# Kernel tuning notes

Measured on AMD Instinct MI355X. Metric: run time of the kernel, lower is better.

## Reference

```python
import jax, jax.numpy as jnp
import numpy as np
from jax import lax

D, NH, T, DFF, SD = 8, 4, 60, 2048, 17
DH = D // NH
NEG = -1e9

def _ln(x, g, b, eps=1e-5):
    m = jnp.mean(x, -1, keepdims=True)
    v = jnp.mean((x - m) ** 2, -1, keepdims=True)
    return (x - m) / jnp.sqrt(v + eps) * g + b

def _mha(q_in, k_in, v_in, Wqkv, bqkv, Wo, bo, mask):
    Wq, Wk, Wv = jnp.split(Wqkv, 3, axis=0)
    bq, bk, bv = jnp.split(bqkv, 3)
    def proj(x, W, bb):
        B, S, _ = x.shape
        return (x @ W.T + bb).reshape(B, S, NH, DH).transpose(0, 2, 1, 3)
    q = proj(q_in, Wq, bq); k = proj(k_in, Wk, bk); v = proj(v_in, Wv, bv)
    s = jnp.einsum('bhqd,bhkd->bhqk', q, k) / np.float32(np.sqrt(DH))
    s = jnp.where(mask, NEG, s)
    o = jnp.einsum('bhqk,bhkd->bhqd', jax.nn.softmax(s, axis=-1), v)
    B, _, S, _ = o.shape
    return o.transpose(0, 2, 1, 3).reshape(B, S, D) @ Wo.T + bo

def _ffn(x, W1, b1, W2, b2):
    return jax.nn.relu(x @ W1.T + b1) @ W2.T + b2

def _forward(x, emb_W, emb_b, eqW, eqb, eoW, eob, ef1W, ef1b, ef2W, ef2b, el1g, el1b, el2g, el2b, eng, enb, dsqW, dsqb, dsoW, dsob, dcqW, dcqb, dcoW, dcob, df1W, df1b, df2W, df2b, dl1g, dl1b, dl2g, dl2b, dl3g, dl3b, dng, dnb, fc_W, fc_b):
    B = x.shape[0]
    idx = jnp.arange(T)
    causal = (idx[None, :] > idx[:, None])[None, None]  # [1,1,T,T], True = blocked

    @jax.checkpoint
    def step(buf, t):
        keymask = (idx > t)[None, None, None, :]  # positions beyond t are padding
        mem = buf
        for i in range(6):  # nn.Transformer default encoder layers
            mem = _ln(mem + _mha(mem, mem, mem, eqW[i], eqb[i], eoW[i], eob[i], keymask), el1g[i], el1b[i])
            mem = _ln(mem + _ffn(mem, ef1W[i], ef1b[i], ef2W[i], ef2b[i]), el2g[i], el2b[i])
        mem = _ln(mem, eng, enb)
        y = buf
        for i in range(2):  # decoder layers
            y = _ln(y + _mha(y, y, y, dsqW[i], dsqb[i], dsoW[i], dsob[i], causal), dl1g[i], dl1b[i])
            y = _ln(y + _mha(y, mem, mem, dcqW[i], dcqb[i], dcoW[i], dcob[i], keymask), dl2g[i], dl2b[i])
            y = _ln(y + _ffn(y, df1W[i], df1b[i], df2W[i], df2b[i]), dl3g[i], dl3b[i])
        y = _ln(y, dng, dnb)
        st = jnp.take(y, t, axis=1) @ fc_W.T + fc_b  # decoded state at last valid pos [B,17]
        buf = buf.at[:, t + 1].set(st @ emb_W.T + emb_b, mode='drop')
        return buf, st

    buf0 = jnp.zeros((B, T, D), x.dtype).at[:, 0].set(x)
    _, states = lax.scan(step, buf0, idx)
    return jnp.transpose(states, (1, 0, 2))  # [B, T, state_dim]

def setup_inputs() -> dict:
    B = 128
    keys = iter(jax.random.split(jax.random.key(0), 64))
    def W(shape):
        return jax.random.normal(next(keys), shape, jnp.float32) / np.float32(np.sqrt(shape[-1]))
    z = lambda *s: jnp.zeros(s, jnp.float32)
    o = lambda *s: jnp.ones(s, jnp.float32)
    return dict(
        quantized_eos_embedding=jax.random.normal(next(keys), (B, D), jnp.float32),
        emb_W=W((D, SD)), emb_b=z(D),
        eqW=W((6, 3 * D, D)), eqb=z(6, 3 * D), eoW=W((6, D, D)), eob=z(6, D),
        ef1W=W((6, DFF, D)), ef1b=z(6, DFF), ef2W=W((6, D, DFF)), ef2b=z(6, D),
        el1g=o(6, D), el1b=z(6, D), el2g=o(6, D), el2b=z(6, D), eng=o(D), enb=z(D),
        dsqW=W((2, 3 * D, D)), dsqb=z(2, 3 * D), dsoW=W((2, D, D)), dsob=z(2, D),
        dcqW=W((2, 3 * D, D)), dcqb=z(2, 3 * D), dcoW=W((2, D, D)), dcob=z(2, D),
        df1W=W((2, DFF, D)), df1b=z(2, DFF), df2W=W((2, D, DFF)), df2b=z(2, D),
        dl1g=o(2, D), dl1b=z(2, D), dl2g=o(2, D), dl2b=z(2, D), dl3g=o(2, D), dl3b=z(2, D),
        dng=o(D), dnb=z(D),
        fc_W=W((SD, D)), fc_b=z(SD),
    )

def reference(quantized_eos_embedding, emb_W, emb_b, eqW, eqb, eoW, eob, ef1W, ef1b, ef2W, ef2b, el1g, el1b, el2g, el2b, eng, enb, dsqW, dsqb, dsoW, dsob, dcqW, dcqb, dcoW, dcob, df1W, df1b, df2W, df2b, dl1g, dl1b, dl2g, dl2b, dl3g, dl3b, dng, dnb, fc_W, fc_b):
    return _forward(quantized_eos_embedding, emb_W, emb_b, eqW, eqb, eoW, eob, ef1W, ef1b, ef2W, ef2b, el1g, el1b, el2g, el2b, eng, enb, dsqW, dsqb, dsoW, dsob, dcqW, dcqb, dcoW, dcob, df1W, df1b, df2W, df2b, dl1g, dl1b, dl2g, dl2b, dl3g, dl3b, dng, dnb, fc_W, fc_b)
```

## Files before the change

### kernel.cpp

```cpp
#include <hip/hip_runtime.h>


typedef __attribute__((ext_vector_type(8))) short short8;
typedef __attribute__((ext_vector_type(4))) float floatx4;
typedef __attribute__((ext_vector_type(4))) unsigned uint4v;

#define DEV static __device__ __forceinline__

namespace {
constexpr int D   = 8;
constexpr int T   = 60;
constexpr int DFF = 2048;
constexpr int SD  = 17;
constexpr int NT  = 512;
constexpr int NW  = NT / 64;
constexpr int NBLK = DFF / 32;
constexpr int BPW  = NBLK / NW;
constexpr int LSTR = NBLK * 2048;
}

struct Params { const float* in[39]; float* out; };

DEV unsigned short f2bf(float f) {
  unsigned u = __builtin_bit_cast(unsigned, f);
  return (unsigned short)((u + 0x8000u) >> 16);
}
DEV float bf2f(unsigned short h) {
  unsigned u = ((unsigned)h) << 16;
  return __builtin_bit_cast(float, u);
}
DEV floatx4 mfma16(short8 a, short8 b, floatx4 c) {
  return __builtin_amdgcn_mfma_f32_16x16x32_bf16(a, b, c, 0, 0, 0);
}
DEV unsigned cvtpk(float lo, float hi) {
  unsigned r;
  asm("v_cvt_pk_bf16_f32 %0, %1, %2" : "=v"(r) : "v"(lo), "v"(hi));
  return r;
}
DEV float lo2f(unsigned u) { return __builtin_bit_cast(float, u << 16); }
DEV float hi2f(unsigned u) { return __builtin_bit_cast(float, u & 0xffff0000u); }
DEV short8 pack4(unsigned a, unsigned b, unsigned c, unsigned d) {
  uint4v u = {a, b, c, d};
  return __builtin_bit_cast(short8, u);
}

__global__ __launch_bounds__(64) void repack_kernel(Params P, short* ws) {
  const int wg = blockIdx.x;
  const int L = wg >> 6, blk = wg & 63;
  const int l = (int)threadIdx.x, gg = l >> 4, rr = l & 15;
  const float *W1p, *b1p, *W2p;
  if (L < 6) { W1p = P.in[7] + L * 16384;  b1p = P.in[8] + L * 2048;  W2p = P.in[9] + L * 16384; }
  else { int m = L - 6; W1p = P.in[25] + m * 16384; b1p = P.in[26] + m * 2048; W2p = P.in[27] + m * 16384; }
  short* out = ws + (L * 64 + blk) * 2048;
  const int j0 = blk * 32;
  short8 z = {0,0,0,0,0,0,0,0};
  for (int tt = 0; tt < 2; ++tt) {
    int j = j0 + tt * 16 + rr;
    short8 r = z;
    if (gg == 3) {
      unsigned short h = f2bf(b1p[j]);
      r[0] = (short)h; r[1] = (short)f2bf(b1p[j] - bf2f(h));
    } else {
      const float* p = W1p + j * 8;
#pragma unroll
      for (int i = 0; i < 8; ++i) {
        float v = p[i];
        unsigned short h = f2bf(v);
        r[i] = (short)((gg == 1) ? f2bf(v - bf2f(h)) : h);
      }
    }
    *(short8*)(out + tt * 512 + l * 8) = r;
  }
  short8 wh = z, wl = z;
  if (rr < 8) {
#pragma unroll
    for (int i = 0; i < 8; ++i) {
      int j = j0 + (i < 4 ? gg * 4 + i : 16 + gg * 4 + (i - 4));
      float v = W2p[rr * 2048 + j];
      unsigned short h = f2bf(v);
      wh[i] = (short)h;
      wl[i] = (short)f2bf(v - bf2f(h));
    }
  }
  *(short8*)(out + 1024 + l * 8) = wh;
  *(short8*)(out + 1536 + l * 8) = wl;
}

__global__ __launch_bounds__(NT, 2) void tdec_kernel(Params P, const short* ws) {
  const int b    = blockIdx.x;
  const int tid  = (int)threadIdx.x;
  const int lane = tid & 63;
  const int wave = tid >> 6;
  const int gg   = lane >> 4;
  const int rr   = lane & 15;

  __shared__ float buf[T][D];
  __shared__ __align__(16) float X[64][D];
  __shared__ float Mem[64][D];
  __shared__ float Qs[64][D];
  __shared__ float Ks[64][D];
  __shared__ float Vs[64][D];
  __shared__ float ATT[64][D];
  __shared__ __align__(16) float red[NW * 1024];
  __shared__ float wAll[10 * 288];
  __shared__ float lnp[40][D];
  __shared__ float b2all[8][D];
  __shared__ float fcw[SD][D];
  __shared__ float fcbv[SD];
  __shared__ float embw[D][SD];
  __shared__ float embbv[D];
  __shared__ float stv[SD];

  for (int o = tid; o < 2880; o += NT) {
    int a = o / 288, off = o - a * 288;
    const float *Wq, *Bq, *Wo, *Bo; int li;
    if (a < 6)              { li = a;            Wq=P.in[3];  Bq=P.in[4];  Wo=P.in[5];  Bo=P.in[6];  }
    else if (((a - 6) & 1) == 0) { li = (a-6)>>1; Wq=P.in[17]; Bq=P.in[18]; Wo=P.in[19]; Bo=P.in[20]; }
    else                    { li = (a-6)>>1;     Wq=P.in[21]; Bq=P.in[22]; Wo=P.in[23]; Bo=P.in[24]; }
    float v;
    if (off < 192)      v = Wq[li*192 + off];
    else if (off < 216) v = Bq[li*24  + off - 192];
    else if (off < 280) v = Wo[li*64  + off - 216];
    else                v = Bo[li*8   + off - 280];
    wAll[o] = v;
  }
  for (int o = tid; o < 320; o += NT) {
    int row = o >> 3, k = o & 7;
    const float* src;
    if (row < 24) { int li = row >> 2, w = row & 3;
      src = (w==0 ? P.in[11] : w==1 ? P.in[12] : w==2 ? P.in[13] : P.in[14]) + li*8;
    } else if (row < 26) src = (row == 24 ? P.in[15] : P.in[16]);
    else if (row < 38) { int q = row - 26, li = q / 6, w = q - li*6;
      src = (w==0?P.in[29]:w==1?P.in[30]:w==2?P.in[31]:w==3?P.in[32]:w==4?P.in[33]:P.in[34]) + li*8;
    } else src = (row == 38 ? P.in[35] : P.in[36]);
    lnp[row][k] = src[k];
  }
  if (tid < 64) { int row = tid >> 3, k = tid & 7;
    b2all[row][k] = (row < 6) ? P.in[10][row*8 + k] : P.in[28][(row-6)*8 + k]; }
  if (tid < 136) fcw[tid >> 3][tid & 7] = P.in[37][tid];
  if (tid < SD)  fcbv[tid] = P.in[38][tid];
  if (tid < 136) embw[tid / 17][tid % 17] = P.in[1][tid];
  if (tid < D)   embbv[tid] = P.in[2][tid];
  if (tid < D)   buf[0][tid] = P.in[0][b*D + tid];
  __syncthreads();

  const short8 zero8 = {0,0,0,0,0,0,0,0};
  const floatx4 zf4  = {0.f,0.f,0.f,0.f};

  auto proj8 = [&](float (*dst)[D], const float (*src)[D], const float* w,
                   const float* bias, int R) {
    for (int o = tid; o < (R << 3); o += NT) {
      int r = o >> 3, d = o & 7;
      const float* wr = w + d * 8;
      const float* xr = src[r];
      float s = bias[d];
#pragma unroll
      for (int k = 0; k < 8; ++k) s += xr[k] * wr[k];
      dst[r][d] = s;
    }
  };

  auto attn = [&](int R, bool causal) {
    int p = tid >> 3, h2 = ((tid >> 1) & 3) << 1, e = tid & 1;
    if (p < R) {
      float q0 = Qs[p][h2]     * 0.70710678118654752f;
      float q1 = Qs[p][h2 + 1] * 0.70710678118654752f;
      int lim = causal ? p : (R - 1);
      float l = 0.f, a0 = 0.f, a1 = 0.f;
      for (int j = e; j <= lim; j += 2) {
        float s = q0 * Ks[j][h2] + q1 * Ks[j][h2 + 1] - 10.f;
        float ev = __expf(s);
        l += ev; a0 += ev * Vs[j][h2]; a1 += ev * Vs[j][h2 + 1];
      }
      l  += __shfl_xor(l, 1);
      a0 += __shfl_xor(a0, 1);
      a1 += __shfl_xor(a1, 1);
      if (e == 0) {
        float rl = 1.f / l;
        ATT[p][h2] = a0 * rl; ATT[p][h2 + 1] = a1 * rl;
      }
    }
  };

  auto oproj_ln = [&](const float* wo, const float* bo, const float* g,
                      const float* bb, int R) {
    if (tid < R) {
      float o[8];
#pragma unroll
      for (int d = 0; d < 8; ++d) {
        float s = bo[d] + X[tid][d];
#pragma unroll
        for (int k = 0; k < 8; ++k) s += ATT[tid][k] * wo[d * 8 + k];
        o[d] = s;
      }
      float m = 0.f;
#pragma unroll
      for (int k = 0; k < 8; ++k) m += o[k];
      m *= 0.125f;
      float v = 0.f;
#pragma unroll
      for (int k = 0; k < 8; ++k) { float dm = o[k] - m; v += dm * dm; }
      float rs = rsqrtf(v * 0.125f + 1e-5f);
#pragma unroll
      for (int k = 0; k < 8; ++k) X[tid][k] = (o[k] - m) * rs * g[k] + bb[k];
    }
  };

  auto ln_rows = [&](float (*dst)[D], const float (*src)[D], const float* g,
                     const float* bb, int R) {
    if (tid < R) {
      float o[8];
#pragma unroll
      for (int k = 0; k < 8; ++k) o[k] = src[tid][k];
      float m = 0.f;
#pragma unroll
      for (int k = 0; k < 8; ++k) m += o[k];
      m *= 0.125f;
      float v = 0.f;
#pragma unroll
      for (int k = 0; k < 8; ++k) { float dm = o[k] - m; v += dm * dm; }
      float rs = rsqrtf(v * 0.125f + 1e-5f);
#pragma unroll
      for (int k = 0; k < 8; ++k) dst[tid][k] = (o[k] - m) * rs * g[k] + bb[k];
    }
  };

  auto mha = [&](int a, float (*kvsrc)[D], bool causal, int R,
                 const float* g, const float* bb) {
    const float* wq = &wAll[a * 288];
    proj8(Qs, X,     wq +   0, wq + 192, R);
    proj8(Ks, kvsrc, wq +  64, wq + 200, R);
    proj8(Vs, kvsrc, wq + 128, wq + 208, R);
    __syncthreads();
    attn(R, causal);
    __syncthreads();
    oproj_ln(wq + 216, wq + 280, g, bb, R);
    __syncthreads();
  };

  auto ffn = [&](const short* wsL, const float* b2, const float* g,
                 const float* bb, int R, int Mt) {
    const short* pb = wsL + (wave * BPW) * 2048;
    short8 a0  = *(const short8*)(pb + lane * 8);
    short8 a1  = *(const short8*)(pb + 512 + lane * 8);
    short8 w2h = *(const short8*)(pb + 1024 + lane * 8);
    short8 w2l = *(const short8*)(pb + 1536 + lane * 8);

    short8 bx[4];
#pragma unroll
    for (int mt = 0; mt < 4; ++mt) {
      short8 v = zero8;
      if (mt < Mt) {
        if (gg == 3) { v[0] = (short)0x3F80; v[1] = (short)0x3F80; }
        else {
          int r = mt * 16 + rr;
          float4 A = *(const float4*)&X[r][0];
          float4 Bv = *(const float4*)&X[r][4];
          unsigned u0 = cvtpk(A.x, A.y), u1 = cvtpk(A.z, A.w);
          unsigned u2 = cvtpk(Bv.x, Bv.y), u3 = cvtpk(Bv.z, Bv.w);
          if (gg == 2) {
            unsigned l0 = cvtpk(A.x - lo2f(u0), A.y - hi2f(u0));
            unsigned l1 = cvtpk(A.z - lo2f(u1), A.w - hi2f(u1));
            unsigned l2 = cvtpk(Bv.x - lo2f(u2), Bv.y - hi2f(u2));
            unsigned l3 = cvtpk(Bv.z - lo2f(u3), Bv.w - hi2f(u3));
            v = pack4(l0, l1, l2, l3);
          } else {
            v = pack4(u0, u1, u2, u3);
          }
        }
      }
      bx[mt] = v;
    }

    floatx4 acc[4] = {zf4, zf4, zf4, zf4};
    for (int blkI = 0; blkI < BPW; ++blkI) {
      short8 na0 = zero8, na1 = zero8, nw2h = zero8, nw2l = zero8;
      if (blkI + 1 < BPW) {
        const short* pn = pb + (blkI + 1) * 2048;
        na0  = *(const short8*)(pn + lane * 8);
        na1  = *(const short8*)(pn + 512 + lane * 8);
        nw2h = *(const short8*)(pn + 1024 + lane * 8);
        nw2l = *(const short8*)(pn + 1536 + lane * 8);
      }
#pragma unroll
      for (int mt = 0; mt < 4; ++mt) {
        if (mt < Mt) {
          floatx4 h0 = mfma16(a0, bx[mt], zf4);
          floatx4 h1 = mfma16(a1, bx[mt], zf4);
          float v0 = fmaxf(h0[0], 0.f), v1 = fmaxf(h0[1], 0.f);
          float v2 = fmaxf(h0[2], 0.f), v3 = fmaxf(h0[3], 0.f);
          float v4 = fmaxf(h1[0], 0.f), v5 = fmaxf(h1[1], 0.f);
          float v6 = fmaxf(h1[2], 0.f), v7 = fmaxf(h1[3], 0.f);
          unsigned u0 = cvtpk(v0, v1), u1 = cvtpk(v2, v3);
          unsigned u2 = cvtpk(v4, v5), u3 = cvtpk(v6, v7);
          unsigned l0 = cvtpk(v0 - lo2f(u0), v1 - hi2f(u0));
          unsigned l1 = cvtpk(v2 - lo2f(u1), v3 - hi2f(u1));
          unsigned l2 = cvtpk(v4 - lo2f(u2), v5 - hi2f(u2));
          unsigned l3 = cvtpk(v6 - lo2f(u3), v7 - hi2f(u3));
          short8 ah = pack4(u0, u1, u2, u3);
          short8 al = pack4(l0, l1, l2, l3);
          acc[mt] = mfma16(w2h, ah, acc[mt]);
          acc[mt] = mfma16(w2h, al, acc[mt]);
          acc[mt] = mfma16(w2l, ah, acc[mt]);
        }
      }
      a0 = na0; a1 = na1; w2h = nw2h; w2l = nw2l;
    }

#pragma unroll
    for (int mt = 0; mt < 4; ++mt)
      if (mt < Mt)
        *(floatx4*)&red[(((wave << 2) + mt) << 8) + (lane << 2)] = acc[mt];
    __syncthreads();
    if (tid < R) {
      int r = tid, mt = r >> 4, rl = r & 15;
      float o[8];
#pragma unroll
      for (int d = 0; d < 8; ++d) {
        float s = X[r][d] + b2[d];
        int base = (mt << 8) + ((((d >> 2) << 4) + rl) << 2) + (d & 3);
#pragma unroll
        for (int w = 0; w < NW; ++w) s += red[(w << 10) + base];
        o[d] = s;
      }
      float m = 0.f;
#pragma unroll
      for (int k = 0; k < 8; ++k) m += o[k];
      m *= 0.125f;
      float var = 0.f;
#pragma unroll
      for (int k = 0; k < 8; ++k) { float dm = o[k] - m; var += dm * dm; }
      float rs = rsqrtf(var * 0.125f + 1e-5f);
#pragma unroll
      for (int k = 0; k < 8; ++k) X[r][k] = (o[k] - m) * rs * g[k] + bb[k];
    }
    __syncthreads();
  };

  for (int t = 0; t < T; ++t) {
    const int R = t + 1;
    const int Mt = (R + 15) >> 4;

    for (int o = tid; o < 512; o += NT) {
      int r = o >> 3, d = o & 7;
      X[r][d] = (r < R) ? buf[r][d] : 0.f;
    }
    __syncthreads();

    for (int li = 0; li < 6; ++li) {
      mha(li, X, false, R, lnp[li * 4 + 0], lnp[li * 4 + 1]);
      ffn(ws + li * LSTR, b2all[li], lnp[li * 4 + 2], lnp[li * 4 + 3], R, Mt);
    }
    ln_rows(X, X, lnp[24], lnp[25], R);
    __syncthreads();
    for (int o = tid; o < 512; o += NT) {
      int r = o >> 3, d = o & 7;
      if (r < R) Mem[r][d] = X[r][d];
      X[r][d] = (r < R) ? buf[r][d] : 0.f;
    }
    __syncthreads();

    for (int li = 0; li < 2; ++li) {
      mha(6 + li * 2, X,   true,  R, lnp[26 + li * 6 + 0], lnp[26 + li * 6 + 1]);
      mha(7 + li * 2, Mem, false, R, lnp[26 + li * 6 + 2], lnp[26 + li * 6 + 3]);
      ffn(ws + (6 + li) * LSTR, b2all[6 + li],
          lnp[26 + li * 6 + 4], lnp[26 + li * 6 + 5], R, Mt);
    }
    ln_rows(X, X, lnp[38], lnp[39], R);
    __syncthreads();

    if (tid < SD) {
      float s = fcbv[tid];
#pragma unroll
      for (int k = 0; k < 8; ++k) s += X[t][k] * fcw[tid][k];
      stv[tid] = s;
      P.out[(b * T + t) * SD + tid] = s;
    }
    __syncthreads();
    if (t + 1 < T && tid < D) {
      float s = embbv[tid];
#pragma unroll
      for (int k = 0; k < SD; ++k) s += stv[k] * embw[tid][k];
      buf[t + 1][tid] = s;
    }
    __syncthreads();
  }
}

extern "C" void kernel_launch(void* const* d_in, const int* in_sizes, int n_in,
                              void* d_out, int out_size, void* d_ws, size_t ws_size,
                              hipStream_t stream) {
  (void)in_sizes; (void)n_in; (void)ws_size; (void)out_size;
  Params P;
  for (int i = 0; i < 39; ++i) P.in[i] = (const float*)d_in[i];
  P.out = (float*)d_out;
  short* ws = (short*)d_ws;
  repack_kernel<<<dim3(8 * NBLK), dim3(64), 0, stream>>>(P, ws);
  tdec_kernel<<<dim3(128), dim3(NT), 0, stream>>>(P, ws);
}
```

Baseline: 3.659 ms.

## Compute final decoder layer only for the last valid row

Only row t of the decoder output is read, so the second decoder layer now computes the query, attention, output projection, FFN and final layernorm for that single row. Keys and values are still projected for all rows. The attention kernel also spreads each query across four lanes instead of two when there are at most 32 rows, to use idle threads. The cost is extra specialised code paths. The time saved is limited because the six encoder layers and the first decoder layer still process every row.

```diff
diff --git a/kernel.cpp b/kernel.cpp
--- a/kernel.cpp
+++ b/kernel.cpp
@@ -161,23 +161,45 @@
   };
 
   auto attn = [&](int R, bool causal) {
-    int p = tid >> 3, h2 = ((tid >> 1) & 3) << 1, e = tid & 1;
-    if (p < R) {
-      float q0 = Qs[p][h2]     * 0.70710678118654752f;
-      float q1 = Qs[p][h2 + 1] * 0.70710678118654752f;
-      int lim = causal ? p : (R - 1);
-      float l = 0.f, a0 = 0.f, a1 = 0.f;
-      for (int j = e; j <= lim; j += 2) {
-        float s = q0 * Ks[j][h2] + q1 * Ks[j][h2 + 1] - 10.f;
-        float ev = __expf(s);
-        l += ev; a0 += ev * Vs[j][h2]; a1 += ev * Vs[j][h2 + 1];
-      }
-      l  += __shfl_xor(l, 1);
-      a0 += __shfl_xor(a0, 1);
-      a1 += __shfl_xor(a1, 1);
-      if (e == 0) {
-        float rl = 1.f / l;
-        ATT[p][h2] = a0 * rl; ATT[p][h2 + 1] = a1 * rl;
+    if (R <= 32) {
+      int p = tid >> 4, h2 = ((tid >> 2) & 3) << 1, e = tid & 3;
+      if (p < R) {
+        float q0 = Qs[p][h2]     * 0.70710678118654752f;
+        float q1 = Qs[p][h2 + 1] * 0.70710678118654752f;
+        int lim = causal ? p : (R - 1);
+        float l = 0.f, a0 = 0.f, a1 = 0.f;
+        for (int j = e; j <= lim; j += 4) {
+          float s = q0 * Ks[j][h2] + q1 * Ks[j][h2 + 1] - 10.f;
+          float ev = __expf(s);
+          l += ev; a0 += ev * Vs[j][h2]; a1 += ev * Vs[j][h2 + 1];
+        }
+        l  += __shfl_xor(l, 1);  l  += __shfl_xor(l, 2);
+        a0 += __shfl_xor(a0, 1); a0 += __shfl_xor(a0, 2);
+        a1 += __shfl_xor(a1, 1); a1 += __shfl_xor(a1, 2);
+        if (e == 0) {
+          float rl = 1.f / l;
+          ATT[p][h2] = a0 * rl; ATT[p][h2 + 1] = a1 * rl;
+        }
+      }
+    } else {
+      int p = tid >> 3, h2 = ((tid >> 1) & 3) << 1, e = tid & 1;
+      if (p < R) {
+        float q0 = Qs[p][h2]     * 0.70710678118654752f;
+        float q1 = Qs[p][h2 + 1] * 0.70710678118654752f;
+        int lim = causal ? p : (R - 1);
+        float l = 0.f, a0 = 0.f, a1 = 0.f;
+        for (int j = e; j <= lim; j += 2) {
+          float s = q0 * Ks[j][h2] + q1 * Ks[j][h2 + 1] - 10.f;
+          float ev = __expf(s);
+          l += ev; a0 += ev * Vs[j][h2]; a1 += ev * Vs[j][h2 + 1];
+        }
+        l  += __shfl_xor(l, 1);
+        a0 += __shfl_xor(a0, 1);
+        a1 += __shfl_xor(a1, 1);
+        if (e == 0) {
+          float rl = 1.f / l;
+          ATT[p][h2] = a0 * rl; ATT[p][h2 + 1] = a1 * rl;
+        }
       }
     }
   };
@@ -235,6 +257,62 @@
     attn(R, causal);
     __syncthreads();
     oproj_ln(wq + 216, wq + 280, g, bb, R);
+    __syncthreads();
+  };
+
+  auto mha_row = [&](int a, float (*kvsrc)[D], int R, int t,
+                     const float* g, const float* bb) {
+    const float* wq = &wAll[a * 288];
+    proj8(Ks, kvsrc, wq +  64, wq + 200, R);
+    proj8(Vs, kvsrc, wq + 128, wq + 208, R);
+    if (tid < 8) {
+      int d = tid;
+      const float* wr = wq + d * 8;
+      float s = wq[192 + d];
+#pragma unroll
+      for (int k = 0; k < 8; ++k) s += X[t][k] * wr[k];
+      Qs[t][d] = s;
+    }
+    __syncthreads();
+    if (tid < 32) {
+      int h2 = (tid >> 3) << 1, e = tid & 7;
+      float q0 = Qs[t][h2]     * 0.70710678118654752f;
+      float q1 = Qs[t][h2 + 1] * 0.70710678118654752f;
+      float l = 0.f, a0 = 0.f, a1 = 0.f;
+      for (int j = e; j < R; j += 8) {
+        float s = q0 * Ks[j][h2] + q1 * Ks[j][h2 + 1] - 10.f;
+        float ev = __expf(s);
+        l += ev; a0 += ev * Vs[j][h2]; a1 += ev * Vs[j][h2 + 1];
+      }
+      l  += __shfl_xor(l, 1);  l  += __shfl_xor(l, 2);  l  += __shfl_xor(l, 4);
+      a0 += __shfl_xor(a0, 1); a0 += __shfl_xor(a0, 2); a0 += __shfl_xor(a0, 4);
+      a1 += __shfl_xor(a1, 1); a1 += __shfl_xor(a1, 2); a1 += __shfl_xor(a1, 4);
+      if (e == 0) {
+        float rl = 1.f / l;
+        ATT[t][h2] = a0 * rl; ATT[t][h2 + 1] = a1 * rl;
+      }
+    }
+    __syncthreads();
+    if (tid == 0) {
+      float o[8];
+#pragma unroll
+      for (int d = 0; d < 8; ++d) {
+        float s = wq[280 + d] + X[t][d];
+#pragma unroll
+        for (int k = 0; k < 8; ++k) s += ATT[t][k] * wq[216 + d * 8 + k];
+        o[d] = s;
+      }
+      float m = 0.f;
+#pragma unroll
+      for (int k = 0; k < 8; ++k) m += o[k];
+      m *= 0.125f;
+      float v = 0.f;
+#pragma unroll
+      for (int k = 0; k < 8; ++k) { float dm = o[k] - m; v += dm * dm; }
+      float rs = rsqrtf(v * 0.125f + 1e-5f);
+#pragma unroll
+      for (int k = 0; k < 8; ++k) X[t][k] = (o[k] - m) * rs * g[k] + bb[k];
+    }
     __syncthreads();
   };
 
@@ -337,6 +415,88 @@
     __syncthreads();
   };
 
+  auto ffn_row = [&](const short* wsL, const float* b2, const float* g,
+                     const float* bb, int t) {
+    const short* pb = wsL + (wave * BPW) * 2048;
+    short8 a0  = *(const short8*)(pb + lane * 8);
+    short8 a1  = *(const short8*)(pb + 512 + lane * 8);
+    short8 w2h = *(const short8*)(pb + 1024 + lane * 8);
+    short8 w2l = *(const short8*)(pb + 1536 + lane * 8);
+
+    short8 bx = zero8;
+    if (gg == 3) { bx[0] = (short)0x3F80; bx[1] = (short)0x3F80; }
+    else if (rr == 0) {
+      float4 A = *(const float4*)&X[t][0];
+      float4 Bv = *(const float4*)&X[t][4];
+      unsigned u0 = cvtpk(A.x, A.y), u1 = cvtpk(A.z, A.w);
+      unsigned u2 = cvtpk(Bv.x, Bv.y), u3 = cvtpk(Bv.z, Bv.w);
+      if (gg == 2) {
+        unsigned l0 = cvtpk(A.x - lo2f(u0), A.y - hi2f(u0));
+        unsigned l1 = cvtpk(A.z - lo2f(u1), A.w - hi2f(u1));
+        unsigned l2 = cvtpk(Bv.x - lo2f(u2), Bv.y - hi2f(u2));
+        unsigned l3 = cvtpk(Bv.z - lo2f(u3), Bv.w - hi2f(u3));
+        bx = pack4(l0, l1, l2, l3);
+      } else {
+        bx = pack4(u0, u1, u2, u3);
+      }
+    }
+
+    floatx4 acc = zf4;
+    for (int blkI = 0; blkI < BPW; ++blkI) {
+      short8 na0 = zero8, na1 = zero8, nw2h = zero8, nw2l = zero8;
+      if (blkI + 1 < BPW) {
+        const short* pn = pb + (blkI + 1) * 2048;
+        na0  = *(const short8*)(pn + lane * 8);
+        na1  = *(const short8*)(pn + 512 + lane * 8);
+        nw2h = *(const short8*)(pn + 1024 + lane * 8);
+        nw2l = *(const short8*)(pn + 1536 + lane * 8);
+      }
+      floatx4 h0 = mfma16(a0, bx, zf4);
+      floatx4 h1 = mfma16(a1, bx, zf4);
+      float v0 = fmaxf(h0[0], 0.f), v1 = fmaxf(h0[1], 0.f);
+      float v2 = fmaxf(h0[2], 0.f), v3 = fmaxf(h0[3], 0.f);
+      float v4 = fmaxf(h1[0], 0.f), v5 = fmaxf(h1[1], 0.f);
+      float v6 = fmaxf(h1[2], 0.f), v7 = fmaxf(h1[3], 0.f);
+      unsigned u0 = cvtpk(v0, v1), u1 = cvtpk(v2, v3);
+      unsigned u2 = cvtpk(v4, v5), u3 = cvtpk(v6, v7);
+      unsigned l0 = cvtpk(v0 - lo2f(u0), v1 - hi2f(u0));
+      unsigned l1 = cvtpk(v2 - lo2f(u1), v3 - hi2f(u1));
+      unsigned l2 = cvtpk(v4 - lo2f(u2), v5 - hi2f(u2));
+      unsigned l3 = cvtpk(v6 - lo2f(u3), v7 - hi2f(u3));
+      short8 ah = pack4(u0, u1, u2, u3);
+      short8 al = pack4(l0, l1, l2, l3);
+      acc = mfma16(w2h, ah, acc);
+      acc = mfma16(w2h, al, acc);
+      acc = mfma16(w2l, ah, acc);
+      a0 = na0; a1 = na1; w2h = nw2h; w2l = nw2l;
+    }
+
+    *(floatx4*)&red[(wave << 10) + (lane << 2)] = acc;
+    __syncthreads();
+    if (tid == 0) {
+      float o[8];
+#pragma unroll
+      for (int d = 0; d < 8; ++d) {
+        float s = X[t][d] + b2[d];
+        int base = ((d >> 2) << 6) + (d & 3);
+#pragma unroll
+        for (int w = 0; w < NW; ++w) s += red[(w << 10) + base];
+        o[d] = s;
+      }
+      float m = 0.f;
+#pragma unroll
+      for (int k = 0; k < 8; ++k) m += o[k];
+      m *= 0.125f;
+      float var = 0.f;
+#pragma unroll
+      for (int k = 0; k < 8; ++k) { float dm = o[k] - m; var += dm * dm; }
+      float rs = rsqrtf(var * 0.125f + 1e-5f);
+#pragma unroll
+      for (int k = 0; k < 8; ++k) X[t][k] = (o[k] - m) * rs * g[k] + bb[k];
+    }
+    __syncthreads();
+  };
+
   for (int t = 0; t < T; ++t) {
     const int R = t + 1;
     const int Mt = (R + 15) >> 4;
@@ -360,15 +520,30 @@
     }
     __syncthreads();
 
-    for (int li = 0; li < 2; ++li) {
-      mha(6 + li * 2, X,   true,  R, lnp[26 + li * 6 + 0], lnp[26 + li * 6 + 1]);
-      mha(7 + li * 2, Mem, false, R, lnp[26 + li * 6 + 2], lnp[26 + li * 6 + 3]);
-      ffn(ws + (6 + li) * LSTR, b2all[6 + li],
-          lnp[26 + li * 6 + 4], lnp[26 + li * 6 + 5], R, Mt);
-    }
-    ln_rows(X, X, lnp[38], lnp[39], R);
-    __syncthreads();
-
+    mha(6, X,   true,  R, lnp[26], lnp[27]);
+    mha(7, Mem, false, R, lnp[28], lnp[29]);
+    ffn(ws + 6 * LSTR, b2all[6], lnp[30], lnp[31], R, Mt);
+
+    mha_row(8, X,   R, t, lnp[32], lnp[33]);
+    mha_row(9, Mem, R, t, lnp[34], lnp[35]);
+    ffn_row(ws + 7 * LSTR, b2all[7], lnp[36], lnp[37], t);
+
+    if (tid == 0) {
+      float o[8];
+#pragma unroll
+      for (int k = 0; k < 8; ++k) o[k] = X[t][k];
+      float m = 0.f;
+#pragma unroll
+      for (int k = 0; k < 8; ++k) m += o[k];
+      m *= 0.125f;
+      float v = 0.f;
+#pragma unroll
+      for (int k = 0; k < 8; ++k) { float dm = o[k] - m; v += dm * dm; }
+      float rs = rsqrtf(v * 0.125f + 1e-5f);
+#pragma unroll
+      for (int k = 0; k < 8; ++k) X[t][k] = (o[k] - m) * rs * lnp[38][k] + lnp[39][k];
+    }
+    __syncthreads();
     if (tid < SD) {
       float s = fcbv[tid];
 #pragma unroll
```

New measurement: 3.473 ms. 1.05x faster.
